# Optimization experiments

Measured on AMD Instinct MI355X. Metric: run time of the kernel, lower is better.

## Reference

```python
import jax, jax.numpy as jnp
import numpy as np

F = 50  # number of feature fields

def setup_inputs() -> dict:
    key = jax.random.key(0)
    k1, k2, k3, k4 = jax.random.split(key, 4)
    B, D, A = 4096, 16, 32
    return {
        "feat_emb": jax.random.normal(k1, (B, F, D), dtype=jnp.float32),
        "W": jax.random.normal(k2, (D, A), dtype=jnp.float32) * 0.1,
        "h": jax.random.normal(k3, (A,), dtype=jnp.float32),
        "p_vec": jax.random.normal(k4, (D,), dtype=jnp.float32),
    }

def reference(feat_emb, W, h, p_vec):
    # build_cross: upper-triangular field pairs (i < j)
    row, col = np.triu_indices(F, k=1)              # each [P], P = F*(F-1)/2
    p = feat_emb[:, row]                             # [B, P, D]
    q = feat_emb[:, col]                             # [B, P, D]
    inter = p * q                                    # pairwise interaction [B, P, D]
    # AttLayer: Dense(no bias) -> relu -> contract with h -> softmax over pairs
    att_signal = jax.nn.relu(jnp.einsum('bpd,da->bpa', inter, W))  # [B, P, A]
    scores = jnp.einsum('bpa,a->bp', att_signal, h)                # [B, P]
    att = jax.nn.softmax(scores, axis=1)                           # [B, P]
    # attention-weighted sum-pooling over pairs
    pooled = jnp.einsum('bp,bpd->bd', att, inter)                  # [B, D]
    # dropout omitted (inference); final projection and reduce
    out = jnp.einsum('bd,d->b', pooled, p_vec)[:, None]            # [B, 1]
    return out
```

## Files before the change

kernel.cpp:

```cpp
#include <hip/hip_runtime.h>
#include <math.h>


#define FF 50
#define DD 16
#define AA 32
#define NP 1225
#define NT32 39
#define ERS 24

typedef _Float16 half8 __attribute__((ext_vector_type(8)));
typedef _Float16 half4 __attribute__((ext_vector_type(4)));
typedef __fp16  fh2   __attribute__((ext_vector_type(2)));
typedef float floatx16 __attribute__((ext_vector_type(16)));

union H8U { half8 v; fh2 h2[4]; };

__global__ __launch_bounds__(256) void afm_kernel(
    const float* __restrict__ feat,
    const float* __restrict__ W,
    const float* __restrict__ h,
    const float* __restrict__ pvec,
    float* __restrict__ out)
{
  __shared__ __align__(16) _Float16 eh[FF * ERS];
  __shared__ unsigned short table[NT32 * 32];
  __shared__ float wred[4][4];

  const int tid    = threadIdx.x;
  const int b      = blockIdx.x;
  const int lane   = tid & 63;
  const int wave   = tid >> 6;
  const int halfid = lane >> 5;
  const int n      = lane & 31;

  if (tid < 200) {
    const float4* src4 = (const float4*)(feat + (size_t)b * (FF * DD));
    float4 v4 = src4[tid];
    int row = tid >> 2, q = tid & 3;
    half4 hv;
    hv[0] = (_Float16)v4.x; hv[1] = (_Float16)v4.y;
    hv[2] = (_Float16)v4.z; hv[3] = (_Float16)v4.w;
    *(half4*)(&eh[row * ERS + q * 4]) = hv;
  }

  for (int p = tid; p < NT32 * 32; p += 256) {
    unsigned short ent = 0;
    if (p < NP) {
      int rad = 9801 - 8 * p;
      int i = (int)((99.0f - sqrtf((float)rad)) * 0.5f);
      if (i < 0) i = 0; if (i > 48) i = 48;
      int off = (i * (99 - i)) >> 1;
      if (off > p) { --i; off = (i * (99 - i)) >> 1; }
      else {
        int off1 = ((i + 1) * (98 - i)) >> 1;
        if (off1 <= p) { ++i; off = off1; }
      }
      int j = p - off + i + 1;
      ent = (unsigned short)((i << 8) | j);
    }
    table[p] = ent;
  }

  half8 A0;
  #pragma unroll
  for (int jj = 0; jj < 8; ++jj)
    A0[jj] = (_Float16)W[(halfid * 8 + jj) * AA + n];
  float hreg[16];
  #pragma unroll
  for (int r = 0; r < 16; ++r)
    hreg[r] = h[(r & 3) + 8 * (r >> 2) + 4 * halfid];
  fh2 pv2[4];
  #pragma unroll
  for (int q = 0; q < 4; ++q) {
    pv2[q][0] = (__fp16)pvec[halfid * 8 + 2 * q];
    pv2[q][1] = (__fp16)pvec[halfid * 8 + 2 * q + 1];
  }
  const floatx16 ZACC = (floatx16)0.0f;

  __syncthreads();

  float m = -3.4e38f, den = 0.f, num = 0.f;
  for (int t = wave; t < NT32; t += 4) {
    const int p  = t * 32 + n;
    const int pk = table[p];
    const int i  = pk >> 8, j = pk & 255;
    H8U Bu;
    {
      half8 Bi = *(const half8*)(&eh[i * ERS + halfid * 8]);
      half8 Bj = *(const half8*)(&eh[j * ERS + halfid * 8]);
      Bu.v = Bi * Bj;
    }
    floatx16 z = __builtin_amdgcn_mfma_f32_32x32x16_f16(A0, Bu.v, ZACC, 0, 0, 0);

    float v = 0.f;
    #pragma unroll
    for (int r = 0; r < 16; ++r)
      v = fmaf(fmaxf(z[r], 0.f), hreg[r], v);
    v += __shfl_xor(v, 32, 64);

    float g;
    {
      float gp = 0.f;
#if __has_builtin(__builtin_amdgcn_fdot2)
      #pragma unroll
      for (int q = 0; q < 4; ++q)
        gp = __builtin_amdgcn_fdot2(Bu.h2[q], pv2[q], gp, false);
#else
      #pragma unroll
      for (int q = 0; q < 4; ++q) {
        gp = fmaf((float)Bu.h2[q][0], (float)pv2[q][0], gp);
        gp = fmaf((float)Bu.h2[q][1], (float)pv2[q][1], gp);
      }
#endif
      g = gp + __shfl_xor(gp, 32, 64);
    }

    if (p >= NP) v = -3.4e38f;
    float mn = fmaxf(m, v);
    float a1 = __expf(m - mn);
    float d1 = __expf(v - mn);
    den = fmaf(den, a1, d1);
    num = fmaf(num, a1, d1 * g);
    m = mn;
  }

  #pragma unroll
  for (int mask = 1; mask <= 16; mask <<= 1) {
    float mo = __shfl_xor(m, mask, 64);
    float dn = __shfl_xor(den, mask, 64);
    float no = __shfl_xor(num, mask, 64);
    float mn = fmaxf(m, mo);
    float a1 = __expf(m - mn), a2 = __expf(mo - mn);
    den = den * a1 + dn * a2;
    num = num * a1 + no * a2;
    m = mn;
  }
  if (lane == 0) { wred[wave][0] = m; wred[wave][1] = den; wred[wave][2] = num; }
  __syncthreads();

  if (tid == 0) {
    float M = -3.4e38f, D = 0.f, N = 0.f;
    #pragma unroll
    for (int w = 0; w < 4; ++w) {
      float wm = wred[w][0], wd = wred[w][1], wn = wred[w][2];
      float mn = fmaxf(M, wm);
      float a1 = __expf(M - mn), a2 = __expf(wm - mn);
      D = D * a1 + wd * a2;
      N = N * a1 + wn * a2;
      M = mn;
    }
    out[b] = N / D;
  }
}

extern "C" void kernel_launch(void* const* d_in, const int* in_sizes, int n_in,
                              void* d_out, int out_size, void* d_ws, size_t ws_size,
                              hipStream_t stream) {
  const float* feat = (const float*)d_in[0];
  const float* W    = (const float*)d_in[1];
  const float* h    = (const float*)d_in[2];
  const float* pvec = (const float*)d_in[3];
  float* out = (float*)d_out;
  const int B = in_sizes[0] / (FF * DD);
  afm_kernel<<<B, 256, 0, stream>>>(feat, W, h, pvec, out);
}
```

Before: 93.20 us.

## Assign one batch row per wave and process two pair tiles per step

Each block now handles four batch rows, one per wave, instead of splitting one row's pair tiles across four waves. This drops the cross-wave shared-memory reduction and the second barrier, and spreads the per-block setup (pair index table, W/h/pvec loads) over four rows. The softmax loop is unrolled by two with one rescale per pair of tiles, uses exp2 with prescaled scores, and splits the accumulators to shorten dependency chains. In exchange each wave runs forty serial tile iterations instead of about ten, the grid is four times smaller, and shared memory per block grows.

```diff
diff --git a/kernel.cpp b/kernel.cpp
--- a/kernel.cpp
+++ b/kernel.cpp
@@ -6,45 +6,50 @@
 #define DD 16
 #define AA 32
 #define NP 1225
-#define NT32 39
+#define NT 40
 #define ERS 24
+#define EBS (FF * ERS)
 
 typedef _Float16 half8 __attribute__((ext_vector_type(8)));
 typedef _Float16 half4 __attribute__((ext_vector_type(4)));
-typedef __fp16  fh2   __attribute__((ext_vector_type(2)));
-typedef float floatx16 __attribute__((ext_vector_type(16)));
+typedef __fp16   fh2   __attribute__((ext_vector_type(2)));
+typedef float    floatx16 __attribute__((ext_vector_type(16)));
 
 union H8U { half8 v; fh2 h2[4]; };
 
-__global__ __launch_bounds__(256) void afm_kernel(
+__global__ __launch_bounds__(256, 4) void afm_kernel(
     const float* __restrict__ feat,
     const float* __restrict__ W,
     const float* __restrict__ h,
     const float* __restrict__ pvec,
-    float* __restrict__ out)
+    float* __restrict__ out,
+    int Btot)
 {
-  __shared__ __align__(16) _Float16 eh[FF * ERS];
-  __shared__ unsigned short table[NT32 * 32];
-  __shared__ float wred[4][4];
+  __shared__ __align__(16) _Float16 eh[4 * EBS];
+  __shared__ unsigned short table[NT * 32];
 
   const int tid    = threadIdx.x;
-  const int b      = blockIdx.x;
   const int lane   = tid & 63;
   const int wave   = tid >> 6;
   const int halfid = lane >> 5;
   const int n      = lane & 31;
+  const int b0     = blockIdx.x << 2;
 
-  if (tid < 200) {
-    const float4* src4 = (const float4*)(feat + (size_t)b * (FF * DD));
-    float4 v4 = src4[tid];
-    int row = tid >> 2, q = tid & 3;
-    half4 hv;
-    hv[0] = (_Float16)v4.x; hv[1] = (_Float16)v4.y;
-    hv[2] = (_Float16)v4.z; hv[3] = (_Float16)v4.w;
-    *(half4*)(&eh[row * ERS + q * 4]) = hv;
+  for (int s = tid; s < 4 * 200; s += 256) {
+    int bl  = s / 200;
+    int rem = s - bl * 200;
+    int bb  = b0 + bl;
+    if (bb < Btot) {
+      float4 v4 = ((const float4*)feat)[(size_t)bb * 200 + rem];
+      half4 hv;
+      hv[0] = (_Float16)v4.x; hv[1] = (_Float16)v4.y;
+      hv[2] = (_Float16)v4.z; hv[3] = (_Float16)v4.w;
+      int row = rem >> 2, q = rem & 3;
+      *(half4*)(&eh[bl * EBS + row * ERS + q * 4]) = hv;
+    }
   }
 
-  for (int p = tid; p < NT32 * 32; p += 256) {
+  for (int p = tid; p < NT * 32; p += 256) {
     unsigned short ent = 0;
     if (p < NP) {
       int rad = 9801 - 8 * p;
@@ -76,82 +81,84 @@
     pv2[q][0] = (__fp16)pvec[halfid * 8 + 2 * q];
     pv2[q][1] = (__fp16)pvec[halfid * 8 + 2 * q + 1];
   }
-  const floatx16 ZACC = (floatx16)0.0f;
 
   __syncthreads();
 
-  float m = -3.4e38f, den = 0.f, num = 0.f;
-  for (int t = wave; t < NT32; t += 4) {
-    const int p  = t * 32 + n;
-    const int pk = table[p];
-    const int i  = pk >> 8, j = pk & 255;
-    H8U Bu;
-    {
-      half8 Bi = *(const half8*)(&eh[i * ERS + halfid * 8]);
-      half8 Bj = *(const half8*)(&eh[j * ERS + halfid * 8]);
-      Bu.v = Bi * Bj;
-    }
-    floatx16 z = __builtin_amdgcn_mfma_f32_32x32x16_f16(A0, Bu.v, ZACC, 0, 0, 0);
+  const _Float16* eb = &eh[wave * EBS];
+  const float LOG2E = 1.4426950408889634f;
+  float m = -3.0e38f, den = 0.f, num = 0.f;
 
-    float v = 0.f;
+  for (int t = 0; t < NT; t += 2) {
+    float vl[2], gg[2];
     #pragma unroll
-    for (int r = 0; r < 16; ++r)
-      v = fmaf(fmaxf(z[r], 0.f), hreg[r], v);
-    v += __shfl_xor(v, 32, 64);
+    for (int u = 0; u < 2; ++u) {
+      const int p  = (t + u) * 32 + n;
+      const int pk = table[p];
+      const int i  = pk >> 8, j = pk & 255;
+      H8U Bu;
+      {
+        half8 Bi = *(const half8*)(eb + i * ERS + halfid * 8);
+        half8 Bj = *(const half8*)(eb + j * ERS + halfid * 8);
+        Bu.v = Bi * Bj;
+      }
+      floatx16 z = __builtin_amdgcn_mfma_f32_32x32x16_f16(
+          A0, Bu.v, (floatx16)0.0f, 0, 0, 0);
 
-    float g;
-    {
-      float gp = 0.f;
+      float a0 = 0.f, a1 = 0.f, a2 = 0.f, a3 = 0.f;
+      #pragma unroll
+      for (int r = 0; r < 16; r += 4) {
+        a0 = fmaf(fmaxf(z[r + 0], 0.f), hreg[r + 0], a0);
+        a1 = fmaf(fmaxf(z[r + 1], 0.f), hreg[r + 1], a1);
+        a2 = fmaf(fmaxf(z[r + 2], 0.f), hreg[r + 2], a2);
+        a3 = fmaf(fmaxf(z[r + 3], 0.f), hreg[r + 3], a3);
+      }
+      float v = (a0 + a1) + (a2 + a3);
+      v += __shfl_xor(v, 32, 64);
+
+      float gp0, gp1;
 #if __has_builtin(__builtin_amdgcn_fdot2)
+      gp0 = __builtin_amdgcn_fdot2(Bu.h2[1], pv2[1],
+            __builtin_amdgcn_fdot2(Bu.h2[0], pv2[0], 0.f, false), false);
+      gp1 = __builtin_amdgcn_fdot2(Bu.h2[3], pv2[3],
+            __builtin_amdgcn_fdot2(Bu.h2[2], pv2[2], 0.f, false), false);
+#else
+      gp0 = 0.f; gp1 = 0.f;
       #pragma unroll
-      for (int q = 0; q < 4; ++q)
-        gp = __builtin_amdgcn_fdot2(Bu.h2[q], pv2[q], gp, false);
-#else
-      #pragma unroll
-      for (int q = 0; q < 4; ++q) {
-        gp = fmaf((float)Bu.h2[q][0], (float)pv2[q][0], gp);
-        gp = fmaf((float)Bu.h2[q][1], (float)pv2[q][1], gp);
+      for (int q = 0; q < 2; ++q) {
+        gp0 = fmaf((float)Bu.h2[q][0], (float)pv2[q][0], gp0);
+        gp0 = fmaf((float)Bu.h2[q][1], (float)pv2[q][1], gp0);
+        gp1 = fmaf((float)Bu.h2[q+2][0], (float)pv2[q+2][0], gp1);
+        gp1 = fmaf((float)Bu.h2[q+2][1], (float)pv2[q+2][1], gp1);
       }
 #endif
-      g = gp + __shfl_xor(gp, 32, 64);
+      float g = gp0 + gp1;
+      g += __shfl_xor(g, 32, 64);
+
+      vl[u] = (p < NP) ? v * LOG2E : -3.0e38f;
+      gg[u] = g;
     }
-
-    if (p >= NP) v = -3.4e38f;
-    float mn = fmaxf(m, v);
-    float a1 = __expf(m - mn);
-    float d1 = __expf(v - mn);
-    den = fmaf(den, a1, d1);
-    num = fmaf(num, a1, d1 * g);
+    float mn = fmaxf(fmaxf(vl[0], vl[1]), m);
+    float a  = exp2f(m - mn);
+    float e0 = exp2f(vl[0] - mn);
+    float e1 = exp2f(vl[1] - mn);
+    den = fmaf(den, a, e0 + e1);
+    num = fmaf(num, a, fmaf(e0, gg[0], e1 * gg[1]));
     m = mn;
   }
 
   #pragma unroll
-  for (int mask = 1; mask <= 16; mask <<= 1) {
+  for (int mask = 16; mask >= 1; mask >>= 1) {
     float mo = __shfl_xor(m, mask, 64);
     float dn = __shfl_xor(den, mask, 64);
     float no = __shfl_xor(num, mask, 64);
     float mn = fmaxf(m, mo);
-    float a1 = __expf(m - mn), a2 = __expf(mo - mn);
-    den = den * a1 + dn * a2;
-    num = num * a1 + no * a2;
+    float s1 = exp2f(m - mn), s2 = exp2f(mo - mn);
+    den = den * s1 + dn * s2;
+    num = num * s1 + no * s2;
     m = mn;
   }
-  if (lane == 0) { wred[wave][0] = m; wred[wave][1] = den; wred[wave][2] = num; }
-  __syncthreads();
-
-  if (tid == 0) {
-    float M = -3.4e38f, D = 0.f, N = 0.f;
-    #pragma unroll
-    for (int w = 0; w < 4; ++w) {
-      float wm = wred[w][0], wd = wred[w][1], wn = wred[w][2];
-      float mn = fmaxf(M, wm);
-      float a1 = __expf(M - mn), a2 = __expf(wm - mn);
-      D = D * a1 + wd * a2;
-      N = N * a1 + wn * a2;
-      M = mn;
-    }
-    out[b] = N / D;
-  }
+  const int b = b0 + wave;
+  if (lane == 0 && b < Btot) out[b] = num / den;
 }
 
 extern "C" void kernel_launch(void* const* d_in, const int* in_sizes, int n_in,
@@ -163,5 +170,5 @@
   const float* pvec = (const float*)d_in[3];
   float* out = (float*)d_out;
   const int B = in_sizes[0] / (FF * DD);
-  afm_kernel<<<B, 256, 0, stream>>>(feat, W, h, pvec, out);
+  afm_kernel<<<(B + 3) / 4, 256, 0, stream>>>(feat, W, h, pvec, out, B);
 }
```

Result: no change. 91.42 us (-1.9%).
